# Optimization experiments

Hardware: AMD Instinct MI355X
Metric: run time of the kernel (lower is better)

Reference implementation:

```python
import jax, jax.numpy as jnp
import numpy as np

V, E, ENC, D, A = 10000, 512, 2048, 512, 512  # vocab, embed, encoder_dim, decoder_dim, attention_dim
B, L, T = 64, 49, 20


def setup_inputs() -> dict:
    key = jax.random.key(0)
    ks = jax.random.split(key, 20)
    s = lambda k, shape, fan: jax.random.normal(k, shape, jnp.float32) / np.sqrt(fan)
    return {
        "encoder_out": jax.random.normal(ks[0], (B, L, ENC), jnp.float32),
        "captions": jax.random.randint(ks[1], (B, T), 0, V),
        "emb_table": s(ks[2], (V, E), E),
        "W_enc_att": s(ks[3], (ENC, A), ENC), "b_enc_att": jnp.zeros((A,), jnp.float32),
        "W_dec_att": s(ks[4], (D, A), D), "b_dec_att": jnp.zeros((A,), jnp.float32),
        "w_full": s(ks[5], (A,), A), "b_full": jnp.zeros((), jnp.float32),
        "W_ih": s(ks[6], (4 * D, E + ENC), E + ENC), "b_ih": jnp.zeros((4 * D,), jnp.float32),
        "W_hh": s(ks[7], (4 * D, D), D), "b_hh": jnp.zeros((4 * D,), jnp.float32),
        "W_init_h": s(ks[8], (ENC, D), ENC), "b_init_h": jnp.zeros((D,), jnp.float32),
        "W_init_c": s(ks[9], (ENC, D), ENC), "b_init_c": jnp.zeros((D,), jnp.float32),
        "W_out": s(ks[10], (D, V), D), "b_out": jnp.zeros((V,), jnp.float32),
    }


def _decoder(encoder_out, captions, emb_table, W_enc_att, b_enc_att, W_dec_att,
             b_dec_att, w_full, b_full, W_ih, b_ih, W_hh, b_hh,
             W_init_h, b_init_h, W_init_c, b_init_c, W_out, b_out):
    # init hidden/cell from mean encoder features
    mean_enc = encoder_out.mean(axis=1)                      # (B, ENC)
    h = mean_enc @ W_init_h + b_init_h                        # (B, D)
    c = mean_enc @ W_init_c + b_init_c
    # precompute encoder projection for additive attention (shared across steps)
    enc_proj = jnp.einsum('ble,ea->bla', encoder_out, W_enc_att) + b_enc_att  # (B, L, A)
    embeddings = emb_table[captions]                          # (B, T, E)
    emb_seq = jnp.swapaxes(embeddings, 0, 1)                  # (T, B, E)
    Dh = h.shape[-1]

    def step(carry, emb_t):
        h, c = carry
        # additive attention over L=49 locations
        dec_proj = h @ W_dec_att + b_dec_att                  # (B, A)
        att = jax.nn.relu(enc_proj + dec_proj[:, None, :])    # (B, L, A)
        scores = jnp.einsum('bla,a->bl', att, w_full) + b_full
        alpha = jax.nn.softmax(scores, axis=-1)               # (B, L)
        context = jnp.einsum('bl,ble->be', alpha, encoder_out)  # (B, ENC)
        # LSTMCell (PyTorch gate order: i, f, g, o)
        x = jnp.concatenate([emb_t, context], axis=1)         # (B, E+ENC)
        gates = x @ W_ih.T + b_ih + h @ W_hh.T + b_hh         # (B, 4D)
        i, f, g, o = jnp.split(gates, 4, axis=1)
        i, f, o = jax.nn.sigmoid(i), jax.nn.sigmoid(f), jax.nn.sigmoid(o)
        g = jnp.tanh(g)
        c_new = f * c + i * g
        h_new = o * jnp.tanh(c_new)
        # dropout is identity in eval mode
        logits_t = h_new @ W_out + b_out                      # (B, V)
        return (h_new, c_new), (logits_t, alpha)

    (_, _), (logits, alphas) = jax.lax.scan(step, (h, c), emb_seq)
    logits = jnp.swapaxes(logits, 0, 1)                       # (B, T, V)
    alphas = jnp.swapaxes(alphas, 0, 1)                       # (B, T, L)
    return logits, alphas


def reference(encoder_out, captions, emb_table, W_enc_att, b_enc_att, W_dec_att,
              b_dec_att, w_full, b_full, W_ih, b_ih, W_hh, b_hh,
              W_init_h, b_init_h, W_init_c, b_init_c, W_out, b_out):
    return _decoder(encoder_out, captions, emb_table, W_enc_att, b_enc_att,
                    W_dec_att, b_dec_att, w_full, b_full, W_ih, b_ih, W_hh, b_hh,
                    W_init_h, b_init_h, W_init_c, b_init_c, W_out, b_out)
```

## Files before the change

kernel.cpp:

```cpp
#include <hip/hip_runtime.h>
#include <hip/hip_bf16.h>

constexpr int NV   = 10000;
constexpr int NE   = 512;
constexpr int NENC = 2048;
constexpr int ND   = 512;
constexpr int NA   = 512;
constexpr int NB   = 64;
constexpr int NL   = 49;
constexpr int NT   = 20;
constexpr int KX   = NE + NENC + ND;
constexpr int KIH  = NE + NENC;

typedef short bfrag __attribute__((ext_vector_type(8)));
typedef float f32x4 __attribute__((ext_vector_type(4)));

__device__ __forceinline__ float us2f(unsigned short u) {
    union { unsigned int i; float f; } x; x.i = (unsigned int)u << 16; return x.f;
}
__device__ __forceinline__ unsigned short f2us(float f) {
    union { float f_; unsigned int u; } x; x.f_ = f;
    unsigned int r = (x.u + 0x7fffu + ((x.u >> 16) & 1u)) >> 16;
    return (unsigned short)r;
}

__launch_bounds__(256)
__global__ void k_mean(const float* __restrict__ enc, unsigned short* __restrict__ meanbf)
{
    const int b = blockIdx.x;
    const int e = blockIdx.y * 256 + threadIdx.x;
    const float* p = enc + (size_t)b * NL * NENC + e;
    float s = 0.f;
    #pragma unroll 7
    for (int l = 0; l < NL; ++l) s += p[(size_t)l * NENC];
    meanbf[(size_t)b * NENC + e] = f2us(s * (1.0f / NL));
}

__launch_bounds__(256)
__global__ void k_init_mfma(const unsigned short* __restrict__ meanbf,
                            const unsigned short* __restrict__ WicT,
                            const float* __restrict__ bh, const float* __restrict__ bc,
                            unsigned short* __restrict__ hbf, float* __restrict__ c)
{
    const int wave = threadIdx.x >> 6, lane = threadIdx.x & 63;
    const int m0 = wave * 16, n0 = blockIdx.x * 16;
    const int r = lane & 15, quad = lane >> 4;
    const unsigned short* ap = meanbf + (size_t)(m0 + r) * NENC + quad * 8;
    const unsigned short* bp = WicT   + (size_t)(n0 + r) * NENC + quad * 8;
    f32x4 acc = {0.f, 0.f, 0.f, 0.f};
    #pragma unroll 8
    for (int k = 0; k < NENC; k += 32) {
        bfrag a = *(const bfrag*)(ap + k);
        bfrag b = *(const bfrag*)(bp + k);
        acc = __builtin_amdgcn_mfma_f32_16x16x32_bf16(a, b, acc, 0, 0, 0);
    }
    const int n = n0 + r;
    const bool isC = n >= ND;
    const float bv = isC ? bc[n - ND] : bh[n];
    #pragma unroll
    for (int i = 0; i < 4; ++i) {
        int m = m0 + quad * 4 + i;
        float v = acc[i] + bv;
        if (isC) c[(size_t)m * ND + (n - ND)] = v;
        else     hbf[(size_t)m * ND + n] = f2us(v);
    }
}

__launch_bounds__(256)
__global__ void k_cvt(const float* __restrict__ src, unsigned short* __restrict__ dst, int n)
{
    int i = (blockIdx.x * 256 + threadIdx.x) * 4;
    if (i < n) {
        float4 v = *(const float4*)(src + i);
        dst[i + 0] = f2us(v.x); dst[i + 1] = f2us(v.y);
        dst[i + 2] = f2us(v.z); dst[i + 3] = f2us(v.w);
    }
}

__launch_bounds__(256)
__global__ void k_transpose(const float* __restrict__ src, unsigned short* __restrict__ dst,
                            int K, int N)
{
    __shared__ float t[32][33];
    const int nb = blockIdx.x * 32, kb = blockIdx.y * 32;
    const int tx = threadIdx.x & 31, ty = threadIdx.x >> 5;
    #pragma unroll
    for (int i = ty; i < 32; i += 8) {
        int n = nb + tx;
        t[i][tx] = (n < N) ? src[(size_t)(kb + i) * N + n] : 0.f;
    }
    __syncthreads();
    #pragma unroll
    for (int i = ty; i < 32; i += 8) {
        int n = nb + i;
        if (n < N) dst[(size_t)n * K + kb + tx] = f2us(t[tx][i]);
    }
}

__launch_bounds__(256)
__global__ void k_encproj_mfma(const unsigned short* __restrict__ encb,
                               const unsigned short* __restrict__ WeaT,
                               const float* __restrict__ bias,
                               unsigned short* __restrict__ epb)
{
    const int j = (blockIdx.x & 7) * 49 + (blockIdx.x >> 3);
    const int ng = j & 7;
    const int mg = j >> 3;
    const int wave = threadIdx.x >> 6, lane = threadIdx.x & 63;
    const int wm = wave >> 1, wn = wave & 1;
    const int m0 = mg * 64 + wm * 32;
    const int n0 = ng * 64 + wn * 32;
    const int r = lane & 15, quad = lane >> 4;
    const unsigned short* ap0 = encb + (size_t)(m0 + r) * NENC + quad * 8;
    const unsigned short* ap1 = ap0 + (size_t)16 * NENC;
    const unsigned short* bp0 = WeaT + (size_t)(n0 + r) * NENC + quad * 8;
    const unsigned short* bp1 = bp0 + (size_t)16 * NENC;
    f32x4 acc00 = {0.f,0.f,0.f,0.f}, acc01 = {0.f,0.f,0.f,0.f};
    f32x4 acc10 = {0.f,0.f,0.f,0.f}, acc11 = {0.f,0.f,0.f,0.f};
    #pragma unroll 4
    for (int k = 0; k < NENC; k += 32) {
        bfrag a0 = *(const bfrag*)(ap0 + k);
        bfrag a1 = *(const bfrag*)(ap1 + k);
        bfrag b0 = *(const bfrag*)(bp0 + k);
        bfrag b1 = *(const bfrag*)(bp1 + k);
        acc00 = __builtin_amdgcn_mfma_f32_16x16x32_bf16(a0, b0, acc00, 0, 0, 0);
        acc01 = __builtin_amdgcn_mfma_f32_16x16x32_bf16(a0, b1, acc01, 0, 0, 0);
        acc10 = __builtin_amdgcn_mfma_f32_16x16x32_bf16(a1, b0, acc10, 0, 0, 0);
        acc11 = __builtin_amdgcn_mfma_f32_16x16x32_bf16(a1, b1, acc11, 0, 0, 0);
    }
    const float bv0 = bias[n0 + r], bv1 = bias[n0 + 16 + r];
    #pragma unroll
    for (int i = 0; i < 4; ++i) {
        int ma = m0 + quad * 4 + i, mb = ma + 16;
        epb[(size_t)ma * NA + n0 + r]      = f2us(acc00[i] + bv0);
        epb[(size_t)ma * NA + n0 + 16 + r] = f2us(acc01[i] + bv1);
        epb[(size_t)mb * NA + n0 + r]      = f2us(acc10[i] + bv0);
        epb[(size_t)mb * NA + n0 + 16 + r] = f2us(acc11[i] + bv1);
    }
}

__device__ __forceinline__ void logits_tasks(int t, int lo, int hi,
    int worker, int nworkers, int wave, int lane,
    const unsigned short* hbf, const unsigned short* WoutT,
    const float* bout, float* out)
{
    const int slot = wave >> 2, w4 = wave & 3;
    const int r = lane & 15, quad = lane >> 4;
    const int m0 = w4 * 16;
    for (int task = lo + worker * 2 + slot; task < hi; task += nworkers * 2) {
        const int n0 = task * 16;
        const unsigned short* ap = hbf + (size_t)(m0 + r) * ND + quad * 8;
        const unsigned short* bp = WoutT + (size_t)(n0 + r) * ND + quad * 8;
        f32x4 acc = {0.f, 0.f, 0.f, 0.f};
        #pragma unroll
        for (int k = 0; k < ND; k += 32) {
            bfrag a = *(const bfrag*)(ap + k);
            bfrag b = *(const bfrag*)(bp + k);
            acc = __builtin_amdgcn_mfma_f32_16x16x32_bf16(a, b, acc, 0, 0, 0);
        }
        const float bv = bout[n0 + r];
        #pragma unroll
        for (int i = 0; i < 4; ++i) {
            int m = m0 + quad * 4 + i;
            out[((size_t)m * NT + t) * NV + n0 + r] = acc[i] + bv;
        }
    }
}

__device__ __forceinline__ void att_half(int t, int b, int half, int tid,
    const unsigned short* hbf, const float* dpg, const unsigned short* epb,
    const unsigned short* encb, const float* wf, const float* bfs,
    const float* embt, const int* caps, unsigned short* x, float* alpha_out,
    float* dp , float* al )
{
    if (half == 0) {
        const int tok = caps[b * NT + t];
        x[(size_t)b * KX + tid] = f2us(embt[(size_t)tok * NE + tid]);
    } else {
        x[(size_t)b * KX + NE + NENC + tid] = hbf[(size_t)b * ND + tid];
    }
    dp[tid] = dpg[(size_t)b * NA + tid];
    __syncthreads();

    const int wave = tid >> 6, lane = tid & 63;
    const float bfull = bfs[0];
    for (int l = wave; l < NL; l += 8) {
        const unsigned short* ep = epb + ((size_t)b * NL + l) * NA;
        float s = 0.f;
        #pragma unroll
        for (int a = lane; a < NA; a += 64) {
            float v = us2f(ep[a]) + dp[a];
            v = v > 0.f ? v : 0.f;
            s = fmaf(v, wf[a], s);
        }
        #pragma unroll
        for (int off = 32; off > 0; off >>= 1) s += __shfl_down(s, off, 64);
        if (lane == 0) al[l] = s + bfull;
    }
    __syncthreads();

    if (tid < 64) {
        float v = (tid < NL) ? al[tid] : -1e30f;
        float m = v;
        #pragma unroll
        for (int off = 32; off > 0; off >>= 1) m = fmaxf(m, __shfl_xor(m, off, 64));
        float e = (tid < NL) ? expf(v - m) : 0.f;
        float s = e;
        #pragma unroll
        for (int off = 32; off > 0; off >>= 1) s += __shfl_xor(s, off, 64);
        float a = e / s;
        if (tid < NL) {
            al[tid] = a;
            if (half == 0) alpha_out[((size_t)b * NT + t) * NL + tid] = a;
        }
    }
    __syncthreads();

    {
        const int e = half * 1024 + tid * 2;
        const unsigned short* p = encb + (size_t)b * NL * NENC + e;
        float s0 = 0.f, s1 = 0.f;
        #pragma unroll 7
        for (int l = 0; l < NL; ++l) {
            ushort2 v = *(const ushort2*)(p + (size_t)l * NENC);
            float a = al[l];
            s0 = fmaf(a, us2f(v.x), s0);
            s1 = fmaf(a, us2f(v.y), s1);
        }
        unsigned short* xo = x + (size_t)b * KX + NE + e;
        xo[0] = f2us(s0); xo[1] = f2us(s1);
    }
}

__launch_bounds__(512)
__global__ void k_att_logits(int t,
                             const unsigned short* __restrict__ hbf,
                             const float* __restrict__ dpg,
                             const unsigned short* __restrict__ epb,
                             const unsigned short* __restrict__ encb,
                             const float* __restrict__ wf,
                             const float* __restrict__ bfs,
                             const float* __restrict__ embt,
                             const int* __restrict__ captions,
                             unsigned short* __restrict__ x,
                             float* __restrict__ alpha_out,
                             const unsigned short* __restrict__ WoutT,
                             const float* __restrict__ bout,
                             float* __restrict__ out)
{
    __shared__ float smem[576];
    const int bid = blockIdx.x, tid = threadIdx.x;
    if (bid < 128) {
        att_half(t, bid >> 1, bid & 1, tid, hbf, dpg, epb, encb, wf, bfs,
                 embt, captions, x, alpha_out, smem, smem + 512);
    } else if (t > 0) {
        logits_tasks(t - 1, 0, 625, bid - 128, 313, tid >> 6, tid & 63,
                     hbf, WoutT, bout, out);
    }
}

__launch_bounds__(512)
__global__ void k_gates_lstm(const unsigned short* __restrict__ x,
                             const unsigned short* __restrict__ Wihb,
                             const unsigned short* __restrict__ Whhb,
                             const float* __restrict__ bih, const float* __restrict__ bhh,
                             unsigned short* __restrict__ hbf, float* __restrict__ c)
{
    __shared__ float part[7 * 4 * 16 * 16];
    const int wave = threadIdx.x >> 6, lane = threadIdx.x & 63;
    const int ng = blockIdx.x & 31, mt = blockIdx.x >> 5;
    const int m0 = mt * 16, n0 = ng * 16;
    const int r = lane & 15, quad = lane >> 4;
    const int k0 = wave * (KX / 8), k1 = k0 + (KX / 8);

    const unsigned short* ap = x + (size_t)(m0 + r) * KX + quad * 8;
    const unsigned short* bpih[4];
    const unsigned short* bphh[4];
    #pragma unroll
    for (int g = 0; g < 4; ++g) {
        bpih[g] = Wihb + (size_t)(g * ND + n0 + r) * KIH + quad * 8;
        bphh[g] = Whhb + (size_t)(g * ND + n0 + r) * ND + quad * 8;
    }
    f32x4 acc[4] = {{0.f,0.f,0.f,0.f},{0.f,0.f,0.f,0.f},
                    {0.f,0.f,0.f,0.f},{0.f,0.f,0.f,0.f}};

    const int kiA = (k1 < KIH) ? k1 : KIH;
    #pragma unroll 4
    for (int k = k0; k < kiA; k += 32) {
        bfrag a = *(const bfrag*)(ap + k);
        #pragma unroll
        for (int g = 0; g < 4; ++g) {
            bfrag b = *(const bfrag*)(bpih[g] + k);
            acc[g] = __builtin_amdgcn_mfma_f32_16x16x32_bf16(a, b, acc[g], 0, 0, 0);
        }
    }
    const int kiB = (k0 > KIH) ? k0 : KIH;
    #pragma unroll 4
    for (int k = kiB; k < k1; k += 32) {
        bfrag a = *(const bfrag*)(ap + k);
        #pragma unroll
        for (int g = 0; g < 4; ++g) {
            bfrag b = *(const bfrag*)(bphh[g] + (k - KIH));
            acc[g] = __builtin_amdgcn_mfma_f32_16x16x32_bf16(a, b, acc[g], 0, 0, 0);
        }
    }

    if (wave > 0) {
        #pragma unroll
        for (int g = 0; g < 4; ++g)
            #pragma unroll
            for (int i = 0; i < 4; ++i)
                part[(((wave - 1) * 4 + g) * 16 + quad * 4 + i) * 16 + r] = acc[g][i];
    }
    __syncthreads();
    if (wave == 0) {
        #pragma unroll
        for (int g = 0; g < 4; ++g)
            #pragma unroll
            for (int i = 0; i < 4; ++i) {
                float v = acc[g][i];
                #pragma unroll
                for (int w = 0; w < 7; ++w)
                    v += part[((w * 4 + g) * 16 + quad * 4 + i) * 16 + r];
                acc[g][i] = v;
            }
        const int d = n0 + r;
        const float b0 = bih[d]        + bhh[d];
        const float b1 = bih[d + 512]  + bhh[d + 512];
        const float b2 = bih[d + 1024] + bhh[d + 1024];
        const float b3 = bih[d + 1536] + bhh[d + 1536];
        #pragma unroll
        for (int i = 0; i < 4; ++i) {
            const int m = m0 + quad * 4 + i;
            float gi = acc[0][i] + b0;
            float gf = acc[1][i] + b1;
            float gg = acc[2][i] + b2;
            float go = acc[3][i] + b3;
            float ig = 1.f / (1.f + expf(-gi));
            float fg = 1.f / (1.f + expf(-gf));
            float g  = tanhf(gg);
            float og = 1.f / (1.f + expf(-go));
            float cn = fg * c[(size_t)m * ND + d] + ig * g;
            float hn = og * tanhf(cn);
            c[(size_t)m * ND + d] = cn;
            hbf[(size_t)m * ND + d] = f2us(hn);
        }
    }
}

__launch_bounds__(512)
__global__ void k_decproj(const unsigned short* __restrict__ hbf,
                          const unsigned short* __restrict__ WdaT,
                          const float* __restrict__ bda, float* __restrict__ dp)
{
    const int wave = threadIdx.x >> 6, lane = threadIdx.x & 63;
    const int slot = wave >> 2, w4 = wave & 3;
    const int tile = blockIdx.x * 2 + slot;
    const int n0 = tile * 16, m0 = w4 * 16;
    const int r = lane & 15, quad = lane >> 4;
    const unsigned short* ap = hbf + (size_t)(m0 + r) * ND + quad * 8;
    const unsigned short* bp = WdaT + (size_t)(n0 + r) * ND + quad * 8;
    f32x4 acc = {0.f, 0.f, 0.f, 0.f};
    #pragma unroll
    for (int k = 0; k < ND; k += 32) {
        bfrag a = *(const bfrag*)(ap + k);
        bfrag b = *(const bfrag*)(bp + k);
        acc = __builtin_amdgcn_mfma_f32_16x16x32_bf16(a, b, acc, 0, 0, 0);
    }
    const float bv = bda[n0 + r];
    #pragma unroll
    for (int i = 0; i < 4; ++i) {
        int m = m0 + quad * 4 + i;
        dp[(size_t)m * NA + n0 + r] = acc[i] + bv;
    }
}

__launch_bounds__(512)
__global__ void k_logits_fin(int t,
                             const unsigned short* __restrict__ hbf,
                             const unsigned short* __restrict__ WoutT,
                             const float* __restrict__ bout,
                             float* __restrict__ out)
{
    logits_tasks(t, 0, 625, blockIdx.x, 313, threadIdx.x >> 6, threadIdx.x & 63,
                 hbf, WoutT, bout, out);
}

extern "C" void kernel_launch(void* const* d_in, const int* in_sizes, int n_in,
                              void* d_out, int out_size, void* d_ws, size_t ws_size,
                              hipStream_t stream) {
    const float* enc  = (const float*)d_in[0];
    const int*   caps = (const int*)d_in[1];
    const float* embt = (const float*)d_in[2];
    const float* Wea  = (const float*)d_in[3];
    const float* bea  = (const float*)d_in[4];
    const float* Wda  = (const float*)d_in[5];
    const float* bda  = (const float*)d_in[6];
    const float* wf   = (const float*)d_in[7];
    const float* bfs  = (const float*)d_in[8];
    const float* Wih  = (const float*)d_in[9];
    const float* bih  = (const float*)d_in[10];
    const float* Whh  = (const float*)d_in[11];
    const float* bhh  = (const float*)d_in[12];
    const float* Wh0  = (const float*)d_in[13];
    const float* bh0  = (const float*)d_in[14];
    const float* Wc0  = (const float*)d_in[15];
    const float* bc0  = (const float*)d_in[16];
    const float* Wout = (const float*)d_in[17];
    const float* bout = (const float*)d_in[18];

    float* out = (float*)d_out;
    float* alpha_out = out + (size_t)NB * NT * NV;

    char* w = (char*)d_ws;
    float* c     = (float*)w;                 w += (size_t)NB * ND * 4;
    float* dp    = (float*)w;                 w += (size_t)NB * NA * 4;
    unsigned short* meanbf = (unsigned short*)w; w += (size_t)NB * NENC * 2;
    unsigned short* hbf   = (unsigned short*)w; w += (size_t)NB * ND * 2;
    unsigned short* x     = (unsigned short*)w; w += (size_t)NB * KX * 2;
    unsigned short* epb   = (unsigned short*)w; w += (size_t)NB * NL * NA * 2;
    unsigned short* encb  = (unsigned short*)w; w += (size_t)NB * NL * NENC * 2;
    unsigned short* Wihb  = (unsigned short*)w; w += (size_t)4 * ND * KIH * 2;
    unsigned short* Whhb  = (unsigned short*)w; w += (size_t)4 * ND * ND * 2;
    unsigned short* WeaT  = (unsigned short*)w; w += (size_t)NA * NENC * 2;
    unsigned short* WdaT  = (unsigned short*)w; w += (size_t)NA * ND * 2;
    unsigned short* WoutT = (unsigned short*)w; w += (size_t)NV * ND * 2;
    unsigned short* WicT  = (unsigned short*)w; w += (size_t)2 * ND * NENC * 2;

    hipLaunchKernelGGL(k_mean, dim3(NB, NENC / 256), dim3(256), 0, stream, enc, meanbf);
    hipLaunchKernelGGL(k_transpose, dim3(ND / 32, NENC / 32), dim3(256), 0, stream,
                       Wh0, WicT, NENC, ND);
    hipLaunchKernelGGL(k_transpose, dim3(ND / 32, NENC / 32), dim3(256), 0, stream,
                       Wc0, WicT + (size_t)ND * NENC, NENC, ND);
    hipLaunchKernelGGL(k_init_mfma, dim3(2 * ND / 16), dim3(256), 0, stream,
                       meanbf, WicT, bh0, bc0, hbf, c);
    {
        int n = NB * NL * NENC;
        hipLaunchKernelGGL(k_cvt, dim3(n / 4 / 256), dim3(256), 0, stream, enc, encb, n);
    }
    {
        int n = 4 * ND * KIH;
        hipLaunchKernelGGL(k_cvt, dim3(n / 4 / 256), dim3(256), 0, stream, Wih, Wihb, n);
    }
    {
        int n = 4 * ND * ND;
        hipLaunchKernelGGL(k_cvt, dim3(n / 4 / 256), dim3(256), 0, stream, Whh, Whhb, n);
    }
    hipLaunchKernelGGL(k_transpose, dim3(NA / 32, NENC / 32), dim3(256), 0, stream,
                       Wea, WeaT, NENC, NA);
    hipLaunchKernelGGL(k_transpose, dim3(NA / 32, ND / 32), dim3(256), 0, stream,
                       Wda, WdaT, ND, NA);
    hipLaunchKernelGGL(k_transpose, dim3((NV + 31) / 32, ND / 32), dim3(256), 0, stream,
                       Wout, WoutT, ND, NV);
    hipLaunchKernelGGL(k_encproj_mfma, dim3((NB * NL / 64) * (NA / 64)), dim3(256), 0, stream,
                       encb, WeaT, bea, epb);
    hipLaunchKernelGGL(k_decproj, dim3(16), dim3(512), 0, stream, hbf, WdaT, bda, dp);

    for (int t = 0; t < NT; ++t) {
        hipLaunchKernelGGL(k_att_logits, dim3(441), dim3(512), 0, stream,
                           t, hbf, dp, epb, encb, wf, bfs, embt, caps, x, alpha_out,
                           WoutT, bout, out);
        hipLaunchKernelGGL(k_gates_lstm, dim3(128), dim3(512), 0, stream,
                           x, Wihb, Whhb, bih, bhh, hbf, c);
        if (t + 1 < NT)
            hipLaunchKernelGGL(k_decproj, dim3(16), dim3(512), 0, stream,
                               hbf, WdaT, bda, dp);
    }
    hipLaunchKernelGGL(k_logits_fin, dim3(313), dim3(512), 0, stream,
                       NT - 1, hbf, WoutT, bout, out);
}
```

Before: 1.156 ms.

## Fold decoder projection into attention kernel and split logits across both step kernels

```diff
diff --git a/kernel.cpp b/kernel.cpp
--- a/kernel.cpp
+++ b/kernel.cpp
@@ -117,17 +117,32 @@
     const unsigned short* bp1 = bp0 + (size_t)16 * NENC;
     f32x4 acc00 = {0.f,0.f,0.f,0.f}, acc01 = {0.f,0.f,0.f,0.f};
     f32x4 acc10 = {0.f,0.f,0.f,0.f}, acc11 = {0.f,0.f,0.f,0.f};
-    #pragma unroll 4
-    for (int k = 0; k < NENC; k += 32) {
-        bfrag a0 = *(const bfrag*)(ap0 + k);
-        bfrag a1 = *(const bfrag*)(ap1 + k);
-        bfrag b0 = *(const bfrag*)(bp0 + k);
-        bfrag b1 = *(const bfrag*)(bp1 + k);
-        acc00 = __builtin_amdgcn_mfma_f32_16x16x32_bf16(a0, b0, acc00, 0, 0, 0);
-        acc01 = __builtin_amdgcn_mfma_f32_16x16x32_bf16(a0, b1, acc01, 0, 0, 0);
-        acc10 = __builtin_amdgcn_mfma_f32_16x16x32_bf16(a1, b0, acc10, 0, 0, 0);
-        acc11 = __builtin_amdgcn_mfma_f32_16x16x32_bf16(a1, b1, acc11, 0, 0, 0);
-    }
+
+    bfrag ca0 = *(const bfrag*)(ap0),      ca1 = *(const bfrag*)(ap1);
+    bfrag cb0 = *(const bfrag*)(bp0),      cb1 = *(const bfrag*)(bp1);
+    bfrag na0 = *(const bfrag*)(ap0 + 32), na1 = *(const bfrag*)(ap1 + 32);
+    bfrag nb0 = *(const bfrag*)(bp0 + 32), nb1 = *(const bfrag*)(bp1 + 32);
+    for (int k = 0; k < NENC - 64; k += 32) {
+        bfrag fa0 = *(const bfrag*)(ap0 + k + 64);
+        bfrag fa1 = *(const bfrag*)(ap1 + k + 64);
+        bfrag fb0 = *(const bfrag*)(bp0 + k + 64);
+        bfrag fb1 = *(const bfrag*)(bp1 + k + 64);
+        acc00 = __builtin_amdgcn_mfma_f32_16x16x32_bf16(ca0, cb0, acc00, 0, 0, 0);
+        acc01 = __builtin_amdgcn_mfma_f32_16x16x32_bf16(ca0, cb1, acc01, 0, 0, 0);
+        acc10 = __builtin_amdgcn_mfma_f32_16x16x32_bf16(ca1, cb0, acc10, 0, 0, 0);
+        acc11 = __builtin_amdgcn_mfma_f32_16x16x32_bf16(ca1, cb1, acc11, 0, 0, 0);
+        ca0 = na0; ca1 = na1; cb0 = nb0; cb1 = nb1;
+        na0 = fa0; na1 = fa1; nb0 = fb0; nb1 = fb1;
+    }
+    acc00 = __builtin_amdgcn_mfma_f32_16x16x32_bf16(ca0, cb0, acc00, 0, 0, 0);
+    acc01 = __builtin_amdgcn_mfma_f32_16x16x32_bf16(ca0, cb1, acc01, 0, 0, 0);
+    acc10 = __builtin_amdgcn_mfma_f32_16x16x32_bf16(ca1, cb0, acc10, 0, 0, 0);
+    acc11 = __builtin_amdgcn_mfma_f32_16x16x32_bf16(ca1, cb1, acc11, 0, 0, 0);
+    acc00 = __builtin_amdgcn_mfma_f32_16x16x32_bf16(na0, nb0, acc00, 0, 0, 0);
+    acc01 = __builtin_amdgcn_mfma_f32_16x16x32_bf16(na0, nb1, acc01, 0, 0, 0);
+    acc10 = __builtin_amdgcn_mfma_f32_16x16x32_bf16(na1, nb0, acc10, 0, 0, 0);
+    acc11 = __builtin_amdgcn_mfma_f32_16x16x32_bf16(na1, nb1, acc11, 0, 0, 0);
+
     const float bv0 = bias[n0 + r], bv1 = bias[n0 + 16 + r];
     #pragma unroll
     for (int i = 0; i < 4; ++i) {
@@ -168,21 +183,40 @@
 }
 
 __device__ __forceinline__ void att_half(int t, int b, int half, int tid,
-    const unsigned short* hbf, const float* dpg, const unsigned short* epb,
-    const unsigned short* encb, const float* wf, const float* bfs,
+    const unsigned short* hcur, const unsigned short* epb,
+    const unsigned short* encb, const unsigned short* WdaT,
+    const float* bda, const float* wf, const float* bfs,
     const float* embt, const int* caps, unsigned short* x, float* alpha_out,
     float* dp , float* al )
 {
+    const int wave = tid >> 6, lane = tid & 63;
+    const int r = lane & 15, quad = lane >> 4;
+
     if (half == 0) {
         const int tok = caps[b * NT + t];
         x[(size_t)b * KX + tid] = f2us(embt[(size_t)tok * NE + tid]);
     } else {
-        x[(size_t)b * KX + NE + NENC + tid] = hbf[(size_t)b * ND + tid];
-    }
-    dp[tid] = dpg[(size_t)b * NA + tid];
+        x[(size_t)b * KX + NE + NENC + tid] = hcur[(size_t)b * ND + tid];
+    }
+
+    {
+        const unsigned short* hb_row = hcur + (size_t)b * ND;
+        #pragma unroll
+        for (int jj = 0; jj < 4; ++jj) {
+            const int n0 = (wave * 4 + jj) * 16;
+            const unsigned short* bp = WdaT + (size_t)(n0 + r) * ND + quad * 8;
+            f32x4 acc = {0.f, 0.f, 0.f, 0.f};
+            #pragma unroll
+            for (int k = 0; k < ND; k += 32) {
+                bfrag a = *(const bfrag*)(hb_row + k + quad * 8);
+                bfrag bb = *(const bfrag*)(bp + k);
+                acc = __builtin_amdgcn_mfma_f32_16x16x32_bf16(a, bb, acc, 0, 0, 0);
+            }
+            if (quad == 0) dp[n0 + r] = acc[0] + bda[n0 + r];
+        }
+    }
     __syncthreads();
 
-    const int wave = tid >> 6, lane = tid & 63;
     const float bfull = bfs[0];
     for (int l = wave; l < NL; l += 8) {
         const unsigned short* ep = epb + ((size_t)b * NL + l) * NA;
@@ -234,10 +268,11 @@
 
 __launch_bounds__(512)
 __global__ void k_att_logits(int t,
-                             const unsigned short* __restrict__ hbf,
-                             const float* __restrict__ dpg,
+                             const unsigned short* __restrict__ hcur,
                              const unsigned short* __restrict__ epb,
                              const unsigned short* __restrict__ encb,
+                             const unsigned short* __restrict__ WdaT,
+                             const float* __restrict__ bda,
                              const float* __restrict__ wf,
                              const float* __restrict__ bfs,
                              const float* __restrict__ embt,
@@ -251,24 +286,37 @@
     __shared__ float smem[576];
     const int bid = blockIdx.x, tid = threadIdx.x;
     if (bid < 128) {
-        att_half(t, bid >> 1, bid & 1, tid, hbf, dpg, epb, encb, wf, bfs,
-                 embt, captions, x, alpha_out, smem, smem + 512);
+        att_half(t, bid >> 1, bid & 1, tid, hcur, epb, encb, WdaT, bda,
+                 wf, bfs, embt, captions, x, alpha_out, smem, smem + 512);
     } else if (t > 0) {
-        logits_tasks(t - 1, 0, 625, bid - 128, 313, tid >> 6, tid & 63,
-                     hbf, WoutT, bout, out);
+        logits_tasks(t - 1, 0, 384, bid - 128, 192, tid >> 6, tid & 63,
+                     hcur, WoutT, bout, out);
     }
 }
 
 __launch_bounds__(512)
-__global__ void k_gates_lstm(const unsigned short* __restrict__ x,
+__global__ void k_gates_lstm(int t,
+                             const unsigned short* __restrict__ x,
                              const unsigned short* __restrict__ Wihb,
                              const unsigned short* __restrict__ Whhb,
                              const float* __restrict__ bih, const float* __restrict__ bhh,
-                             unsigned short* __restrict__ hbf, float* __restrict__ c)
+                             unsigned short* __restrict__ hnxt, float* __restrict__ c,
+                             const unsigned short* __restrict__ hcur,
+                             const unsigned short* __restrict__ WoutT,
+                             const float* __restrict__ bout,
+                             float* __restrict__ out)
 {
     __shared__ float part[7 * 4 * 16 * 16];
+    const int bid = blockIdx.x;
     const int wave = threadIdx.x >> 6, lane = threadIdx.x & 63;
-    const int ng = blockIdx.x & 31, mt = blockIdx.x >> 5;
+    if (bid >= 128) {
+        if (t > 0)
+            logits_tasks(t - 1, 384, 625, bid - 128, 121, wave, lane,
+                         hcur, WoutT, bout, out);
+        return;
+    }
+    const int ng = (bid & 7) * 4 + ((bid >> 3) & 3);
+    const int mt = bid >> 5;
     const int m0 = mt * 16, n0 = ng * 16;
     const int r = lane & 15, quad = lane >> 4;
     const int k0 = wave * (KX / 8), k1 = k0 + (KX / 8);
@@ -343,35 +391,8 @@
             float cn = fg * c[(size_t)m * ND + d] + ig * g;
             float hn = og * tanhf(cn);
             c[(size_t)m * ND + d] = cn;
-            hbf[(size_t)m * ND + d] = f2us(hn);
-        }
-    }
-}
-
-__launch_bounds__(512)
-__global__ void k_decproj(const unsigned short* __restrict__ hbf,
-                          const unsigned short* __restrict__ WdaT,
-                          const float* __restrict__ bda, float* __restrict__ dp)
-{
-    const int wave = threadIdx.x >> 6, lane = threadIdx.x & 63;
-    const int slot = wave >> 2, w4 = wave & 3;
-    const int tile = blockIdx.x * 2 + slot;
-    const int n0 = tile * 16, m0 = w4 * 16;
-    const int r = lane & 15, quad = lane >> 4;
-    const unsigned short* ap = hbf + (size_t)(m0 + r) * ND + quad * 8;
-    const unsigned short* bp = WdaT + (size_t)(n0 + r) * ND + quad * 8;
-    f32x4 acc = {0.f, 0.f, 0.f, 0.f};
-    #pragma unroll
-    for (int k = 0; k < ND; k += 32) {
-        bfrag a = *(const bfrag*)(ap + k);
-        bfrag b = *(const bfrag*)(bp + k);
-        acc = __builtin_amdgcn_mfma_f32_16x16x32_bf16(a, b, acc, 0, 0, 0);
-    }
-    const float bv = bda[n0 + r];
-    #pragma unroll
-    for (int i = 0; i < 4; ++i) {
-        int m = m0 + quad * 4 + i;
-        dp[(size_t)m * NA + n0 + r] = acc[i] + bv;
+            hnxt[(size_t)m * ND + d] = f2us(hn);
+        }
     }
 }
 
@@ -414,9 +435,8 @@
 
     char* w = (char*)d_ws;
     float* c     = (float*)w;                 w += (size_t)NB * ND * 4;
-    float* dp    = (float*)w;                 w += (size_t)NB * NA * 4;
     unsigned short* meanbf = (unsigned short*)w; w += (size_t)NB * NENC * 2;
-    unsigned short* hbf   = (unsigned short*)w; w += (size_t)NB * ND * 2;
+    unsigned short* hb    = (unsigned short*)w; w += (size_t)2 * NB * ND * 2;
     unsigned short* x     = (unsigned short*)w; w += (size_t)NB * KX * 2;
     unsigned short* epb   = (unsigned short*)w; w += (size_t)NB * NL * NA * 2;
     unsigned short* encb  = (unsigned short*)w; w += (size_t)NB * NL * NENC * 2;
@@ -433,7 +453,7 @@
     hipLaunchKernelGGL(k_transpose, dim3(ND / 32, NENC / 32), dim3(256), 0, stream,
                        Wc0, WicT + (size_t)ND * NENC, NENC, ND);
     hipLaunchKernelGGL(k_init_mfma, dim3(2 * ND / 16), dim3(256), 0, stream,
-                       meanbf, WicT, bh0, bc0, hbf, c);
+                       meanbf, WicT, bh0, bc0, hb, c);
     {
         int n = NB * NL * NENC;
         hipLaunchKernelGGL(k_cvt, dim3(n / 4 / 256), dim3(256), 0, stream, enc, encb, n);
@@ -454,18 +474,17 @@
                        Wout, WoutT, ND, NV);
     hipLaunchKernelGGL(k_encproj_mfma, dim3((NB * NL / 64) * (NA / 64)), dim3(256), 0, stream,
                        encb, WeaT, bea, epb);
-    hipLaunchKernelGGL(k_decproj, dim3(16), dim3(512), 0, stream, hbf, WdaT, bda, dp);
 
     for (int t = 0; t < NT; ++t) {
-        hipLaunchKernelGGL(k_att_logits, dim3(441), dim3(512), 0, stream,
-                           t, hbf, dp, epb, encb, wf, bfs, embt, caps, x, alpha_out,
-                           WoutT, bout, out);
-        hipLaunchKernelGGL(k_gates_lstm, dim3(128), dim3(512), 0, stream,
-                           x, Wihb, Whhb, bih, bhh, hbf, c);
-        if (t + 1 < NT)
-            hipLaunchKernelGGL(k_decproj, dim3(16), dim3(512), 0, stream,
-                               hbf, WdaT, bda, dp);
+        unsigned short* hcur = hb + (size_t)(t & 1) * NB * ND;
+        unsigned short* hnxt = hb + (size_t)((t + 1) & 1) * NB * ND;
+        hipLaunchKernelGGL(k_att_logits, dim3(320), dim3(512), 0, stream,
+                           t, hcur, epb, encb, WdaT, bda, wf, bfs, embt, caps,
+                           x, alpha_out, WoutT, bout, out);
+        hipLaunchKernelGGL(k_gates_lstm, dim3(249), dim3(512), 0, stream,
+                           t, x, Wihb, Whhb, bih, bhh, hnxt, c,
+                           hcur, WoutT, bout, out);
     }
     hipLaunchKernelGGL(k_logits_fin, dim3(313), dim3(512), 0, stream,
-                       NT - 1, hbf, WoutT, bout, out);
-}
+                       NT - 1, hb + (size_t)(NT & 1) * NB * ND, WoutT, bout, out);
+}
```

New measurement: 1.298 ms. 1.12x slower.

## Double-buffer hidden state and split previous-step logits across attention and gates kernels

Applied to the files above, without the earlier changes.

```diff
diff --git a/kernel.cpp b/kernel.cpp
--- a/kernel.cpp
+++ b/kernel.cpp
@@ -167,19 +167,19 @@
     }
 }
 
-__device__ __forceinline__ void att_half(int t, int b, int half, int tid,
-    const unsigned short* hbf, const float* dpg, const unsigned short* epb,
+__device__ __forceinline__ void att_body(int t, int b, int tid,
+    const unsigned short* hcur, const float* dpg, const unsigned short* epb,
     const unsigned short* encb, const float* wf, const float* bfs,
     const float* embt, const int* caps, unsigned short* x, float* alpha_out,
     float* dp , float* al )
 {
-    if (half == 0) {
-        const int tok = caps[b * NT + t];
-        x[(size_t)b * KX + tid] = f2us(embt[(size_t)tok * NE + tid]);
-    } else {
-        x[(size_t)b * KX + NE + NENC + tid] = hbf[(size_t)b * ND + tid];
-    }
-    dp[tid] = dpg[(size_t)b * NA + tid];
+    for (int d = tid; d < ND; d += 512)
+        x[(size_t)b * KX + NE + NENC + d] = hcur[(size_t)b * ND + d];
+    for (int a = tid; a < NA; a += 512)
+        dp[a] = dpg[(size_t)b * NA + a];
+    const int tok = caps[b * NT + t];
+    for (int j = tid; j < NE; j += 512)
+        x[(size_t)b * KX + j] = f2us(embt[(size_t)tok * NE + j]);
     __syncthreads();
 
     const int wave = tid >> 6, lane = tid & 63;
@@ -211,30 +211,32 @@
         float a = e / s;
         if (tid < NL) {
             al[tid] = a;
-            if (half == 0) alpha_out[((size_t)b * NT + t) * NL + tid] = a;
+            alpha_out[((size_t)b * NT + t) * NL + tid] = a;
         }
     }
     __syncthreads();
 
     {
-        const int e = half * 1024 + tid * 2;
+        const int e = tid * 4;
         const unsigned short* p = encb + (size_t)b * NL * NENC + e;
-        float s0 = 0.f, s1 = 0.f;
+        float s0 = 0.f, s1 = 0.f, s2 = 0.f, s3 = 0.f;
         #pragma unroll 7
         for (int l = 0; l < NL; ++l) {
-            ushort2 v = *(const ushort2*)(p + (size_t)l * NENC);
+            ushort4 v = *(const ushort4*)(p + (size_t)l * NENC);
             float a = al[l];
             s0 = fmaf(a, us2f(v.x), s0);
             s1 = fmaf(a, us2f(v.y), s1);
+            s2 = fmaf(a, us2f(v.z), s2);
+            s3 = fmaf(a, us2f(v.w), s3);
         }
         unsigned short* xo = x + (size_t)b * KX + NE + e;
-        xo[0] = f2us(s0); xo[1] = f2us(s1);
+        xo[0] = f2us(s0); xo[1] = f2us(s1); xo[2] = f2us(s2); xo[3] = f2us(s3);
     }
 }
 
 __launch_bounds__(512)
 __global__ void k_att_logits(int t,
-                             const unsigned short* __restrict__ hbf,
+                             const unsigned short* __restrict__ hcur,
                              const float* __restrict__ dpg,
                              const unsigned short* __restrict__ epb,
                              const unsigned short* __restrict__ encb,
@@ -250,25 +252,38 @@
 {
     __shared__ float smem[576];
     const int bid = blockIdx.x, tid = threadIdx.x;
-    if (bid < 128) {
-        att_half(t, bid >> 1, bid & 1, tid, hbf, dpg, epb, encb, wf, bfs,
+    if (bid < 64) {
+        att_body(t, bid, tid, hcur, dpg, epb, encb, wf, bfs,
                  embt, captions, x, alpha_out, smem, smem + 512);
     } else if (t > 0) {
-        logits_tasks(t - 1, 0, 625, bid - 128, 313, tid >> 6, tid & 63,
-                     hbf, WoutT, bout, out);
+        logits_tasks(t - 1, 0, 384, bid - 64, 192, tid >> 6, tid & 63,
+                     hcur, WoutT, bout, out);
     }
 }
 
 __launch_bounds__(512)
-__global__ void k_gates_lstm(const unsigned short* __restrict__ x,
+__global__ void k_gates_lstm(int t,
+                             const unsigned short* __restrict__ x,
                              const unsigned short* __restrict__ Wihb,
                              const unsigned short* __restrict__ Whhb,
                              const float* __restrict__ bih, const float* __restrict__ bhh,
-                             unsigned short* __restrict__ hbf, float* __restrict__ c)
+                             unsigned short* __restrict__ hnxt, float* __restrict__ c,
+                             const unsigned short* __restrict__ hcur,
+                             const unsigned short* __restrict__ WoutT,
+                             const float* __restrict__ bout,
+                             float* __restrict__ out)
 {
     __shared__ float part[7 * 4 * 16 * 16];
+    const int bid = blockIdx.x;
     const int wave = threadIdx.x >> 6, lane = threadIdx.x & 63;
-    const int ng = blockIdx.x & 31, mt = blockIdx.x >> 5;
+    if (bid >= 128) {
+        if (t > 0)
+            logits_tasks(t - 1, 384, 625, bid - 128, 121, wave, lane,
+                         hcur, WoutT, bout, out);
+        return;
+    }
+    const int ng = (bid & 7) * 4 + ((bid >> 3) & 3);
+    const int mt = bid >> 5;
     const int m0 = mt * 16, n0 = ng * 16;
     const int r = lane & 15, quad = lane >> 4;
     const int k0 = wave * (KX / 8), k1 = k0 + (KX / 8);
@@ -343,7 +358,7 @@
             float cn = fg * c[(size_t)m * ND + d] + ig * g;
             float hn = og * tanhf(cn);
             c[(size_t)m * ND + d] = cn;
-            hbf[(size_t)m * ND + d] = f2us(hn);
+            hnxt[(size_t)m * ND + d] = f2us(hn);
         }
     }
 }
@@ -416,7 +431,7 @@
     float* c     = (float*)w;                 w += (size_t)NB * ND * 4;
     float* dp    = (float*)w;                 w += (size_t)NB * NA * 4;
     unsigned short* meanbf = (unsigned short*)w; w += (size_t)NB * NENC * 2;
-    unsigned short* hbf   = (unsigned short*)w; w += (size_t)NB * ND * 2;
+    unsigned short* hb    = (unsigned short*)w; w += (size_t)2 * NB * ND * 2;
     unsigned short* x     = (unsigned short*)w; w += (size_t)NB * KX * 2;
     unsigned short* epb   = (unsigned short*)w; w += (size_t)NB * NL * NA * 2;
     unsigned short* encb  = (unsigned short*)w; w += (size_t)NB * NL * NENC * 2;
@@ -433,7 +448,7 @@
     hipLaunchKernelGGL(k_transpose, dim3(ND / 32, NENC / 32), dim3(256), 0, stream,
                        Wc0, WicT + (size_t)ND * NENC, NENC, ND);
     hipLaunchKernelGGL(k_init_mfma, dim3(2 * ND / 16), dim3(256), 0, stream,
-                       meanbf, WicT, bh0, bc0, hbf, c);
+                       meanbf, WicT, bh0, bc0, hb, c);
     {
         int n = NB * NL * NENC;
         hipLaunchKernelGGL(k_cvt, dim3(n / 4 / 256), dim3(256), 0, stream, enc, encb, n);
@@ -454,18 +469,21 @@
                        Wout, WoutT, ND, NV);
     hipLaunchKernelGGL(k_encproj_mfma, dim3((NB * NL / 64) * (NA / 64)), dim3(256), 0, stream,
                        encb, WeaT, bea, epb);
-    hipLaunchKernelGGL(k_decproj, dim3(16), dim3(512), 0, stream, hbf, WdaT, bda, dp);
+    hipLaunchKernelGGL(k_decproj, dim3(16), dim3(512), 0, stream, hb, WdaT, bda, dp);
 
     for (int t = 0; t < NT; ++t) {
-        hipLaunchKernelGGL(k_att_logits, dim3(441), dim3(512), 0, stream,
-                           t, hbf, dp, epb, encb, wf, bfs, embt, caps, x, alpha_out,
-                           WoutT, bout, out);
-        hipLaunchKernelGGL(k_gates_lstm, dim3(128), dim3(512), 0, stream,
-                           x, Wihb, Whhb, bih, bhh, hbf, c);
+        unsigned short* hcur = hb + (size_t)(t & 1) * NB * ND;
+        unsigned short* hnxt = hb + (size_t)((t + 1) & 1) * NB * ND;
+        hipLaunchKernelGGL(k_att_logits, dim3(256), dim3(512), 0, stream,
+                           t, hcur, dp, epb, encb, wf, bfs, embt, caps,
+                           x, alpha_out, WoutT, bout, out);
+        hipLaunchKernelGGL(k_gates_lstm, dim3(249), dim3(512), 0, stream,
+                           t, x, Wihb, Whhb, bih, bhh, hnxt, c,
+                           hcur, WoutT, bout, out);
         if (t + 1 < NT)
             hipLaunchKernelGGL(k_decproj, dim3(16), dim3(512), 0, stream,
-                               hbf, WdaT, bda, dp);
+                               hnxt, WdaT, bda, dp);
     }
     hipLaunchKernelGGL(k_logits_fin, dim3(313), dim3(512), 0, stream,
-                       NT - 1, hbf, WoutT, bout, out);
-}
+                       NT - 1, hb + (size_t)(NT & 1) * NB * ND, WoutT, bout, out);
+}
```

After: 1.038 ms. -10.1%, faster.
